# Performance work log

Measured on AMD Instinct MI355X. Metric: run time of the kernel, lower is better.

## Reference

```python
import jax, jax.numpy as jnp
import numpy as np

C = 0.1            # args.hyp_c
EPS_PROJ = 4e-3    # hyptorch project eps for float32
MIN_NORM = 1e-5
NUM_HEADS = 12


def _norm(x):
    return jnp.maximum(jnp.linalg.norm(x, axis=-1, keepdims=True), MIN_NORM)


def expmap0(u, c):
    sqrt_c = c ** 0.5
    u_norm = _norm(u)
    return jnp.tanh(sqrt_c * u_norm) * u / (sqrt_c * u_norm)


def project(x, c):
    sqrt_c = c ** 0.5
    norm = _norm(x)
    maxnorm = (1.0 - EPS_PROJ) / sqrt_c
    return jnp.where(norm > maxnorm, x / norm * maxnorm, x)


def logmap0(y, c):
    sqrt_c = c ** 0.5
    y_norm = _norm(y)
    arg = jnp.clip(sqrt_c * y_norm, -1 + 1e-5, 1 - 1e-5)
    artanh = 0.5 * jnp.log((1 + arg) / (1 - arg))
    return y / (y_norm * sqrt_c) * artanh


def qkv_attention(x, wq, bq, wk, bk, wv, bv, num_heads):
    # x: [B, N, D]; weights in torch Linear convention [out, in]
    B, N, D = x.shape
    dh = D // num_heads
    q = (x @ wq.T + bq).reshape(B, N, num_heads, dh)
    k = (x @ wk.T + bk).reshape(B, N, num_heads, dh)
    v = (x @ wv.T + bv).reshape(B, N, num_heads, dh)
    # NOTE: original has no 1/sqrt(dh) scaling — keep faithful
    att = jnp.einsum('bnhd,bmhd->bhnm', q, k)
    att = jax.nn.softmax(att, axis=-1)
    out = jnp.einsum('bhnm,bmhd->bnhd', att, v)
    return out.reshape(B, N, D)


def setup_inputs() -> dict:
    key = jax.random.key(0)
    ks = jax.random.split(key, 7)
    B, N, D = 8, 1024, 768
    s = 0.02
    return {
        'x':   jax.random.normal(ks[0], (B, N, D), jnp.float32),
        'w_q': jax.random.normal(ks[1], (3, D, D), jnp.float32) * s,
        'b_q': jax.random.normal(ks[2], (3, D), jnp.float32) * s,
        'w_k': jax.random.normal(ks[3], (3, D, D), jnp.float32) * s,
        'b_k': jax.random.normal(ks[4], (3, D), jnp.float32) * s,
        'w_v': jax.random.normal(ks[5], (3, D, D), jnp.float32) * s,
        'b_v': jax.random.normal(ks[6], (3, D), jnp.float32) * s,
    }


def reference(x, w_q, b_q, w_k, b_k, w_v, b_v):
    # branch 0: euclidean; branch 1: hyperbolic (ToPoincare); branch 2: spherical (FromPoincare)
    x_e = x
    x_h = project(expmap0(x, C), C)
    x_s = logmap0(x, C)
    out = 0.0
    for i, xb in enumerate((x_e, x_h, x_s)):
        out = out + qkv_attention(xb, w_q[i], b_q[i], w_k[i], b_k[i],
                                  w_v[i], b_v[i], NUM_HEADS)
    return out
```

## Files before the change

kernel.cpp:

```cpp
#include <hip/hip_runtime.h>
#include <hip/hip_bf16.h>
#include <cstdint>
#include <cstddef>

#define B_   8
#define N_   1024
#define D_   768
#define H_   12
#define DH_  64
#define M_   (B_ * N_)
#define WSZ_ (D_ * D_)

typedef __bf16 bf16;
typedef bf16  bf16x8  __attribute__((ext_vector_type(8)));
typedef bf16  bf16x4  __attribute__((ext_vector_type(4)));
typedef float floatx4 __attribute__((ext_vector_type(4)));

#define MFMA16 __builtin_amdgcn_mfma_f32_16x16x32_bf16

__device__ __forceinline__ float exp2_fast(float x) {
    float r;
    asm("v_exp_f32 %0, %1" : "=v"(r) : "v"(x));
    return r;
}

__device__ __forceinline__ void gload_lds16(const void* g, void* l) {
    __builtin_amdgcn_global_load_lds(
        (const __attribute__((address_space(1))) unsigned int*)g,
        (__attribute__((address_space(3))) unsigned int*)l, 16, 0, 0);
}

__global__ __launch_bounds__(256) void prep_x(const float* __restrict__ x,
                                              bf16* __restrict__ xbf,
                                              float* __restrict__ sc ) {
    int row = blockIdx.x;
    int tid = threadIdx.x;
    const float* xr = x + (size_t)row * D_;
    bf16* xo = xbf + (size_t)row * D_;
    float v0 = xr[tid], v1 = xr[tid + 256], v2 = xr[tid + 512];
    xo[tid]       = (bf16)v0;
    xo[tid + 256] = (bf16)v1;
    xo[tid + 512] = (bf16)v2;
    float ss = v0 * v0 + v1 * v1 + v2 * v2;
    for (int off = 32; off; off >>= 1) ss += __shfl_xor(ss, off, 64);
    __shared__ float red[4];
    if ((tid & 63) == 0) red[tid >> 6] = ss;
    __syncthreads();
    if (tid == 0) {
        float t2 = red[0] + red[1] + red[2] + red[3];
        float t  = sqrtf(t2);
        const float scst = 0.31622776601683794f;
        float un = fmaxf(t, 1e-5f);
        float s1 = tanhf(scst * un) / (scst * un);
        float nh = fmaxf(t * s1, 1e-5f);
        float maxnorm = (1.0f - 4e-3f) / scst;
        float sh = (nh > maxnorm) ? s1 * (maxnorm / nh) : s1;
        float arg = fminf(scst * un, 1.0f - 1e-5f);
        float artanh = 0.5f * logf((1.0f + arg) / (1.0f - arg));
        float ssc = artanh / (un * scst);
        sc[row]      = sh;
        sc[M_ + row] = ssc;
    }
}

__global__ __launch_bounds__(256) void prep_w(const float* __restrict__ wq,
                                              const float* __restrict__ wk,
                                              const float* __restrict__ wv,
                                              bf16* __restrict__ wbf) {
    size_t i = ((size_t)blockIdx.x * 256 + threadIdx.x) * 4;
    int z = (int)(i / WSZ_);
    int r = (int)(i % WSZ_);
    int branch = z / 3, t = z % 3;
    const float* src = (t == 0 ? wq : t == 1 ? wk : wv) + (size_t)branch * WSZ_ + r;
    float4 f = *(const float4*)src;
    bf16x4 o = { (bf16)f.x, (bf16)f.y, (bf16)f.z, (bf16)f.w };
    *(bf16x4*)(wbf + i) = o;
}

#define NT9 12

#define STG(buf, mat, half, t) do {                                          \
    const bf16* _src = (mat) ? wbf : xbf;                                    \
    int _rb = ((mat) ? bn0 : bm0) + (half) * 128 + w * 16 + (lane >> 2);     \
    const bf16* _g = _src + (size_t)_rb * D_ + (t) * 64 + (lane & 3) * 8;    \
    bf16* _l = &L[buf][mat][half][0][w * 16][0];                             \
    gload_lds16(_g, _l);                                                     \
    gload_lds16(_g + 32, _l + 4096);                                         \
} while (0)

#define LOADA(buf, mh) do {                                                  \
    _Pragma("unroll") for (int fi = 0; fi < 4; fi++)                         \
    _Pragma("unroll") for (int kk = 0; kk < 2; kk++)                         \
        afr[fi][kk] = *(const bf16x8*)(&L[buf][0][wm][kk][(mh)*64 + fi*16 + c15][quad*8]); \
} while (0)

#define LOADB(buf, nh) do {                                                  \
    _Pragma("unroll") for (int fj = 0; fj < 2; fj++)                         \
    _Pragma("unroll") for (int kk = 0; kk < 2; kk++)                         \
        bfr[nh][fj][kk] = *(const bf16x8*)(&L[buf][1][wn>>1][kk][(wn&1)*64 + (nh)*32 + fj*16 + c15][quad*8]); \
} while (0)

#define MFMACL(mh, nh) do {                                                  \
    __builtin_amdgcn_s_setprio(1);                                           \
    _Pragma("unroll") for (int fi = 0; fi < 4; fi++)                         \
    _Pragma("unroll") for (int fj = 0; fj < 2; fj++)                         \
    _Pragma("unroll") for (int kk = 0; kk < 2; kk++)                         \
        acc[(mh)*4 + fi][(nh)*2 + fj] =                                      \
            MFMA16(afr[fi][kk], bfr[nh][fj][kk], acc[(mh)*4 + fi][(nh)*2 + fj], 0, 0, 0); \
    __builtin_amdgcn_s_setprio(0);                                           \
} while (0)

#define BAR() __builtin_amdgcn_s_barrier()
#define VMW4() asm volatile("s_waitcnt vmcnt(4)" ::: "memory")

__global__ __launch_bounds__(512, 2) void gemm_qkv9(
        const bf16* __restrict__ xbf, const bf16* __restrict__ wbf,
        const float* __restrict__ bq, const float* __restrict__ bk,
        const float* __restrict__ bv, const float* __restrict__ sc,
        bf16* __restrict__ qkv) {
    int bid = blockIdx.x;
    int v = (bid & 7) * 108 + (bid >> 3);
    int bx = v >> 5;
    int by = v & 31;
    int bn0 = bx * 256;
    int bm0 = by * 256;

    __shared__ bf16 L[2][2][2][2][128][32];

    int tid = threadIdx.x;
    int w = tid >> 6, lane = tid & 63;
    int wm = w >> 2, wn = w & 3;
    int quad = lane >> 4, c15 = lane & 15;

    bf16x8 afr[4][2];
    bf16x8 bfr[2][2][2];
    floatx4 acc[8][4];
#pragma unroll
    for (int i = 0; i < 8; i++)
#pragma unroll
        for (int j = 0; j < 4; j++) acc[i][j] = (floatx4){0.f, 0.f, 0.f, 0.f};

    STG(0, 0, 0, 0); STG(0, 0, 1, 0); STG(0, 1, 0, 0); STG(0, 1, 1, 0);
    STG(1, 1, 0, 1); STG(1, 1, 1, 1);
    VMW4();
    BAR();

    for (int it = 0; it < 6; it++) {
        int t1 = 2 * it + 1;
        bool st2 = (it < 5);
        LOADA(0, 0); LOADB(0, 0);
        STG(1, 0, 0, t1);
        BAR(); MFMACL(0, 0); BAR();
        LOADB(0, 1);
        STG(1, 0, 1, t1);
        BAR(); MFMACL(0, 1); BAR();
        LOADA(0, 1);
        if (st2) STG(0, 1, 0, t1 + 1);
        BAR(); MFMACL(1, 1); BAR();
        if (st2) STG(0, 1, 1, t1 + 1);
        VMW4();
        BAR(); MFMACL(1, 0); BAR();
        LOADA(1, 0); LOADB(1, 0);
        if (st2) STG(0, 0, 0, t1 + 1);
        BAR(); MFMACL(0, 0); BAR();
        LOADB(1, 1);
        if (st2) STG(0, 0, 1, t1 + 1);
        BAR(); MFMACL(0, 1); BAR();
        LOADA(1, 1);
        if (st2) STG(1, 1, 0, t1 + 2);
        BAR(); MFMACL(1, 1); BAR();
        if (st2) STG(1, 1, 1, t1 + 2);
        VMW4();
        BAR(); MFMACL(1, 0); BAR();
    }

    int gz = bn0 / 768;
    int branch = gz / 3, t = gz % 3;
    int colz0 = (bn0 % 768) + wn * 64;
    const float* bias = (t == 0 ? bq : t == 1 ? bk : bv) + branch * D_;
    const float* scb = (branch == 0) ? nullptr : sc + (size_t)(branch - 1) * M_;
    float bj[4];
#pragma unroll
    for (int fj = 0; fj < 4; fj++) bj[fj] = bias[colz0 + fj * 16 + c15];
    bf16* outz = qkv + (size_t)gz * M_ * D_;
#pragma unroll
    for (int fi = 0; fi < 8; fi++) {
        int rowbase = bm0 + wm * 128 + fi * 16 + quad * 4;
        float4 sv = scb ? *(const float4*)(scb + rowbase)
                        : (float4){1.f, 1.f, 1.f, 1.f};
        float svr[4] = { sv.x, sv.y, sv.z, sv.w };
        if (t == 2) {
            int b = rowbase >> 10, nn = rowbase & 1023;
#pragma unroll
            for (int fj = 0; fj < 4; fj++) {
                int col = colz0 + fj * 16 + c15;
                int h = col >> 6, dd = col & 63;
                bf16x4 pkv;
#pragma unroll
                for (int r = 0; r < 4; r++)
                    pkv[r] = (bf16)(svr[r] * acc[fi][fj][r] + bj[fj]);
                *(bf16x4*)(outz + (((size_t)(b * H_ + h) * 64 + dd) << 10) + nn) = pkv;
            }
        } else {
#pragma unroll
            for (int r = 0; r < 4; r++) {
                bf16* orow = outz + (size_t)(rowbase + r) * D_;
#pragma unroll
                for (int fj = 0; fj < 4; fj++)
                    orow[colz0 + fj * 16 + c15] = (bf16)(svr[r] * acc[fi][fj][r] + bj[fj]);
            }
        }
    }
}

#define BM 128
#define BN 128
#define BK 32
__global__ __launch_bounds__(256) void gemm_qkv(
        const bf16* __restrict__ xbf, const bf16* __restrict__ wbf_all,
        const float* __restrict__ bq, const float* __restrict__ bk,
        const float* __restrict__ bv, const float* __restrict__ sc,
        int zoff, bf16* __restrict__ qkv) {
    int gz = zoff + blockIdx.z;
    int branch = gz / 3, t = gz % 3;
    const bf16*  wsrc = wbf_all + (size_t)gz * WSZ_;
    const float* bias = (t == 0 ? bq : t == 1 ? bk : bv) + branch * D_;
    bf16* out = qkv + (size_t)blockIdx.z * M_ * D_;
    int bm0 = blockIdx.y * BM;
    int bn0 = blockIdx.x * BN;

    __shared__ bf16 lA[BM * BK];
    __shared__ bf16 lB[BN * BK];

    int tid = threadIdx.x;
    int w = tid >> 6, lane = tid & 63;
    int wr = w >> 1, wc = w & 1;
    int quad = lane >> 4, c15 = lane & 15;
    int lrow = lane >> 2;
    int lcol = (lane & 3) * 8;

    floatx4 acc[4][4];
    for (int i = 0; i < 4; i++)
        for (int j = 0; j < 4; j++)
            acc[i][j] = (floatx4){0.f, 0.f, 0.f, 0.f};

    for (int k0 = 0; k0 < D_; k0 += BK) {
        const bf16* ga = xbf  + ((size_t)(bm0 + w * 32 + lrow) * D_ + k0 + lcol);
        const bf16* gb = wsrc + ((size_t)(bn0 + w * 32 + lrow) * D_ + k0 + lcol);
        gload_lds16(ga,           (char*)lA + w * 2048);
        gload_lds16(ga + 16 * D_, (char*)lA + w * 2048 + 1024);
        gload_lds16(gb,           (char*)lB + w * 2048);
        gload_lds16(gb + 16 * D_, (char*)lB + w * 2048 + 1024);
        __syncthreads();

        int arow = wr * 64 + c15;
        int brow = wc * 64 + c15;
        int kq = quad * 8;
        bf16x8 af[4], bfm[4];
        for (int i = 0; i < 4; i++) af[i]  = *(const bf16x8*)(lA + (arow + i * 16) * BK + kq);
        for (int j = 0; j < 4; j++) bfm[j] = *(const bf16x8*)(lB + (brow + j * 16) * BK + kq);
        for (int i = 0; i < 4; i++)
            for (int j = 0; j < 4; j++)
                acc[i][j] = MFMA16(af[i], bfm[j], acc[i][j], 0, 0, 0);
        __syncthreads();
    }

    const float* scb = (branch == 0) ? nullptr : sc + (size_t)(branch - 1) * M_;
    float bj[4];
    for (int j = 0; j < 4; j++) bj[j] = bias[bn0 + wc * 64 + j * 16 + c15];
    for (int i = 0; i < 4; i++) {
        int gRow0 = bm0 + wr * 64 + i * 16 + quad * 4;
        float s[4];
        for (int r = 0; r < 4; r++) s[r] = scb ? scb[gRow0 + r] : 1.0f;
        if (t == 2) {
            int b = gRow0 >> 10, nn = gRow0 & 1023;
            for (int j = 0; j < 4; j++) {
                int col = bn0 + wc * 64 + j * 16 + c15;
                int h = col >> 6, dd = col & 63;
                bf16x4 pkv;
                for (int r = 0; r < 4; r++)
                    pkv[r] = (bf16)(s[r] * acc[i][j][r] + bj[j]);
                *(bf16x4*)(out + (((size_t)(b * H_ + h) * 64 + dd) << 10) + nn) = pkv;
            }
        } else {
            for (int r = 0; r < 4; r++) {
                bf16* orow = out + (size_t)(gRow0 + r) * D_;
                for (int j = 0; j < 4; j++) {
                    int gCol = bn0 + wc * 64 + j * 16 + c15;
                    orow[gCol] = (bf16)(s[r] * acc[i][j][r] + bj[j]);
                }
            }
        }
    }
}

#define LDKP 72
__global__ __launch_bounds__(256) void attn(const bf16* __restrict__ qkv,
                                            float* __restrict__ out) {
    int qt = blockIdx.x;
    int bh = blockIdx.y;
    int br = blockIdx.z;
    int batch = bh / H_, head = bh % H_;
    int n0 = qt * 128;
    int tid = threadIdx.x, w = tid >> 6, lane = tid & 63;
    int quad = lane >> 4, c15 = lane & 15;

    const bf16* base = qkv + (size_t)br * 3 * M_ * D_;
    size_t baseRow = (size_t)batch * N_;
    int colOff = head * DH_;
    const bf16* qb  = base;
    const bf16* kb  = base + (size_t)M_ * D_;
    const bf16* vtb = base + (size_t)2 * M_ * D_
                    + ((size_t)(batch * H_ + head) * 64) * 1024;

    __shared__ bf16 sK[2][64][64];
    __shared__ bf16 sV[2][64][64];
    __shared__ bf16 sP[4][32 * LDKP];
    bf16* sPw = sP[w];

    int lr  = lane >> 3;
    int swz = ((lane & 7) ^ lr) * 8;
    const bf16* kgl = kb  + (baseRow + w * 8 + lr) * D_ + colOff + swz;
    const bf16* vgl = vtb + ((size_t)(w * 8 + lr)) * 1024 + swz;

    int s0 = (quad ^ (c15 & 7)) * 8;
    int s1 = s0 ^ 32;

    bf16x8 aq[2][2];
#pragma unroll
    for (int h = 0; h < 2; h++) {
        const bf16* qp = qb + ((baseRow + n0 + w * 32 + h * 16 + c15) * D_ + colOff + quad * 8);
        aq[h][0] = *(const bf16x8*)qp;
        aq[h][1] = *(const bf16x8*)(qp + 32);
#pragma unroll
        for (int f = 0; f < 2; f++)
#pragma unroll
            for (int i = 0; i < 8; i++)
                aq[h][f][i] = (bf16)((float)aq[h][f][i] * 1.4426950408889634f);
    }

    float m_sw[2] = { 0.f, 0.f };
    float l_sw[2] = { 0.f, 0.f };
    floatx4 o_acc[2][4];
#pragma unroll
    for (int h = 0; h < 2; h++)
#pragma unroll
        for (int j = 0; j < 4; j++) o_acc[h][j] = (floatx4){0.f, 0.f, 0.f, 0.f};

    gload_lds16(kgl,                      &sK[0][w * 8][0]);
    gload_lds16(kgl + (size_t)32 * D_,    &sK[0][32 + w * 8][0]);
    gload_lds16(vgl,                      &sV[0][w * 8][0]);
    gload_lds16(vgl + 32 * 1024,          &sV[0][32 + w * 8][0]);
    asm volatile("s_waitcnt vmcnt(0)" ::: "memory");
    __builtin_amdgcn_s_barrier();

    int buf = 0;
    for (int kt = 0; kt < 16; kt++) {
        if (kt < 15) {
            int m1 = (kt + 1) * 64;
            gload_lds16(kgl + (size_t)m1 * D_,        &sK[buf ^ 1][w * 8][0]);
            gload_lds16(kgl + (size_t)(m1 + 32) * D_, &sK[buf ^ 1][32 + w * 8][0]);
            gload_lds16(vgl + m1,                     &sV[buf ^ 1][w * 8][0]);
            gload_lds16(vgl + 32 * 1024 + m1,         &sV[buf ^ 1][32 + w * 8][0]);
        }

        floatx4 sfr[2][4];
        __builtin_amdgcn_s_setprio(1);
#pragma unroll
        for (int j = 0; j < 4; j++) {
            const bf16* kp = &sK[buf][j * 16 + c15][0];
            bf16x8 k0 = *(const bf16x8*)(kp + s0);
            bf16x8 k1 = *(const bf16x8*)(kp + s1);
#pragma unroll
            for (int h = 0; h < 2; h++) {
                floatx4 z = (floatx4){0.f, 0.f, 0.f, 0.f};
                z = MFMA16(k0, aq[h][0], z, 0, 0, 0);
                z = MFMA16(k1, aq[h][1], z, 0, 0, 0);
                sfr[h][j] = z;
            }
        }
        __builtin_amdgcn_s_setprio(0);

#pragma unroll
        for (int h = 0; h < 2; h++) {
            float q0 = fmaxf(fmaxf(sfr[h][0][0], sfr[h][0][1]), fmaxf(sfr[h][0][2], sfr[h][0][3]));
            float q1 = fmaxf(fmaxf(sfr[h][1][0], sfr[h][1][1]), fmaxf(sfr[h][1][2], sfr[h][1][3]));
            float q2 = fmaxf(fmaxf(sfr[h][2][0], sfr[h][2][1]), fmaxf(sfr[h][2][2], sfr[h][2][3]));
            float q3 = fmaxf(fmaxf(sfr[h][3][0], sfr[h][3][1]), fmaxf(sfr[h][3][2], sfr[h][3][3]));
            float mx = fmaxf(fmaxf(q0, q1), fmaxf(q2, q3));
            if (__any(mx > m_sw[h] + 11.0f)) {
                float mr = fmaxf(mx, __shfl_xor(mx, 16, 64));
                mr = fmaxf(mr, __shfl_xor(mr, 32, 64));
                float mnew = fmaxf(m_sw[h], mr);
                float alpha = exp2_fast(m_sw[h] - mnew);
                l_sw[h] *= alpha;
                m_sw[h] = mnew;
#pragma unroll
                for (int r = 0; r < 4; r++) {
                    float a = __shfl(alpha, quad * 4 + r, 64);
#pragma unroll
                    for (int j = 0; j < 4; j++) o_acc[h][j][r] *= a;
                }
            }
            float m = m_sw[h];
            float pe[4][4];
            bf16x4 pk[4];
#pragma unroll
            for (int j = 0; j < 4; j++)
#pragma unroll
                for (int r = 0; r < 4; r++) {
                    float p = exp2_fast(sfr[h][j][r] - m);
                    pe[j][r] = p;
                    pk[j][r] = (bf16)p;
                }
            float f0 = (pe[0][0] + pe[0][1]) + (pe[0][2] + pe[0][3]);
            float f1 = (pe[1][0] + pe[1][1]) + (pe[1][2] + pe[1][3]);
            float f2 = (pe[2][0] + pe[2][1]) + (pe[2][2] + pe[2][3]);
            float f3 = (pe[3][0] + pe[3][1]) + (pe[3][2] + pe[3][3]);
            float sum = (f0 + f1) + (f2 + f3);
            sum += __shfl_xor(sum, 16, 64);
            sum += __shfl_xor(sum, 32, 64);
            l_sw[h] += sum;
            bf16* pw = sPw + (h * 16 + c15) * LDKP;
#pragma unroll
            for (int j = 0; j < 4; j++)
                *(bf16x4*)(pw + j * 16 + quad * 4) = pk[j];
        }

        asm volatile("s_waitcnt lgkmcnt(0)" ::: "memory");
        __builtin_amdgcn_sched_barrier(0);

        bf16x8 ap[2][2];
#pragma unroll
        for (int h = 0; h < 2; h++) {
            const bf16* pp = sPw + (h * 16 + c15) * LDKP + quad * 8;
            ap[h][0] = *(const bf16x8*)pp;
            ap[h][1] = *(const bf16x8*)(pp + 32);
        }
        __builtin_amdgcn_s_setprio(1);
#pragma unroll
        for (int j = 0; j < 4; j++) {
            const bf16* vp = &sV[buf][j * 16 + c15][0];
            bf16x8 v0 = *(const bf16x8*)(vp + s0);
            bf16x8 v1 = *(const bf16x8*)(vp + s1);
#pragma unroll
            for (int h = 0; h < 2; h++) {
                o_acc[h][j] = MFMA16(ap[h][0], v0, o_acc[h][j], 0, 0, 0);
                o_acc[h][j] = MFMA16(ap[h][1], v1, o_acc[h][j], 0, 0, 0);
            }
        }
        __builtin_amdgcn_s_setprio(0);

        if (kt < 15) {
            asm volatile("s_waitcnt vmcnt(0)" ::: "memory");
            __builtin_amdgcn_s_barrier();
            buf ^= 1;
        }
    }

#pragma unroll
    for (int h = 0; h < 2; h++) {
        float inv = 1.0f / l_sw[h];
#pragma unroll
        for (int r = 0; r < 4; r++) {
            float iv = __shfl(inv, quad * 4 + r, 64);
            int row = n0 + w * 32 + h * 16 + quad * 4 + r;
            float* op = out + ((size_t)batch * N_ + row) * D_ + colOff;
#pragma unroll
            for (int j = 0; j < 4; j++) {
                float v = o_acc[h][j][r] * iv;
                int col = j * 16 + c15;
                unsafeAtomicAdd(op + col, v);
            }
        }
    }
}

extern "C" void kernel_launch(void* const* d_in, const int* in_sizes, int n_in,
                              void* d_out, int out_size, void* d_ws, size_t ws_size,
                              hipStream_t stream) {
    const float* x  = (const float*)d_in[0];
    const float* wq = (const float*)d_in[1];
    const float* bq = (const float*)d_in[2];
    const float* wk = (const float*)d_in[3];
    const float* bk = (const float*)d_in[4];
    const float* wv = (const float*)d_in[5];
    const float* bv = (const float*)d_in[6];
    float* out = (float*)d_out;

    char* ws = (char*)d_ws;
    bf16*  xbf = (bf16*)ws;
    bf16*  wbf = (bf16*)(ws + 12582912);
    float* sc  = (float*)(ws + 12582912 + 10616832);
    bf16*  qkv = (bf16*)(ws + 12582912 + 10616832 + 65536);

    const size_t matB = (size_t)M_ * D_ * 2;
    const size_t need_all = 12582912 + 10616832 + 65536 + 9 * matB;

    hipMemsetAsync(d_out, 0, out_size, stream);
    hipLaunchKernelGGL(prep_x, dim3(M_), dim3(256), 0, stream, x, xbf, sc);
    hipLaunchKernelGGL(prep_w, dim3((9 * WSZ_ / 4) / 256), dim3(256), 0, stream, wq, wk, wv, wbf);

    if (ws_size >= need_all) {
        hipLaunchKernelGGL(gemm_qkv9, dim3(864), dim3(512), 0, stream,
                           xbf, wbf, bq, bk, bv, sc, qkv);
        hipLaunchKernelGGL(attn, dim3(N_ / 128, B_ * H_, 3), dim3(256), 0, stream,
                           qkv, out);
    } else {
        for (int br = 0; br < 3; br++) {
            hipLaunchKernelGGL(gemm_qkv, dim3(D_ / BN, M_ / BM, 3), dim3(256), 0, stream,
                               xbf, wbf, bq, bk, bv, sc, br * 3, qkv);
            hipLaunchKernelGGL(attn, dim3(N_ / 128, B_ * H_, 1), dim3(256), 0, stream,
                               qkv, out);
        }
    }
}
```

Measured before the change: 362.8 us.

## Fuse three attention branches per block, drop memset and atomics

The attention kernel now loops over all three branches inside one block, using a continuous double-buffered K/V pipeline across branch boundaries. It sums the normalized outputs in registers and writes them with plain stores, which removes the output memset and the atomic adds in the main path. Blocks are remapped with an XCD-aware swizzle and launch bounds now request 4 waves per SIMD. prep_x also switches to float4 loads with 192 threads. In exchange, each block runs three times longer with a third as many blocks, and it holds more registers for the extra accumulator.

Result: slower. 385.2 us (+6.2%).

```diff
diff --git a/kernel.cpp b/kernel.cpp
--- a/kernel.cpp
+++ b/kernel.cpp
@@ -30,24 +30,22 @@
         (__attribute__((address_space(3))) unsigned int*)l, 16, 0, 0);
 }
 
-__global__ __launch_bounds__(256) void prep_x(const float* __restrict__ x,
+__global__ __launch_bounds__(192) void prep_x(const float* __restrict__ x,
                                               bf16* __restrict__ xbf,
                                               float* __restrict__ sc ) {
     int row = blockIdx.x;
     int tid = threadIdx.x;
     const float* xr = x + (size_t)row * D_;
-    bf16* xo = xbf + (size_t)row * D_;
-    float v0 = xr[tid], v1 = xr[tid + 256], v2 = xr[tid + 512];
-    xo[tid]       = (bf16)v0;
-    xo[tid + 256] = (bf16)v1;
-    xo[tid + 512] = (bf16)v2;
-    float ss = v0 * v0 + v1 * v1 + v2 * v2;
+    float4 v = *(const float4*)(xr + tid * 4);
+    bf16x4 o = { (bf16)v.x, (bf16)v.y, (bf16)v.z, (bf16)v.w };
+    *(bf16x4*)(xbf + (size_t)row * D_ + tid * 4) = o;
+    float ss = v.x * v.x + v.y * v.y + v.z * v.z + v.w * v.w;
     for (int off = 32; off; off >>= 1) ss += __shfl_xor(ss, off, 64);
-    __shared__ float red[4];
+    __shared__ float red[3];
     if ((tid & 63) == 0) red[tid >> 6] = ss;
     __syncthreads();
     if (tid == 0) {
-        float t2 = red[0] + red[1] + red[2] + red[3];
+        float t2 = red[0] + red[1] + red[2];
         float t  = sqrtf(t2);
         const float scst = 0.31622776601683794f;
         float un = fmaxf(t, 1e-5f);
@@ -295,23 +293,20 @@
 }
 
 #define LDKP 72
-__global__ __launch_bounds__(256) void attn(const bf16* __restrict__ qkv,
-                                            float* __restrict__ out) {
-    int qt = blockIdx.x;
-    int bh = blockIdx.y;
-    int br = blockIdx.z;
+__global__ __launch_bounds__(256, 4) void attn(const bf16* __restrict__ qkv,
+                                               float* __restrict__ out,
+                                               int nbr, int accumulate) {
+    int hwid = blockIdx.x;
+    int lg = (hwid & 7) * 96 + (hwid >> 3);
+    int qt = lg & 7;
+    int bh = lg >> 3;
     int batch = bh / H_, head = bh % H_;
     int n0 = qt * 128;
     int tid = threadIdx.x, w = tid >> 6, lane = tid & 63;
     int quad = lane >> 4, c15 = lane & 15;
 
-    const bf16* base = qkv + (size_t)br * 3 * M_ * D_;
     size_t baseRow = (size_t)batch * N_;
     int colOff = head * DH_;
-    const bf16* qb  = base;
-    const bf16* kb  = base + (size_t)M_ * D_;
-    const bf16* vtb = base + (size_t)2 * M_ * D_
-                    + ((size_t)(batch * H_ + head) * 64) * 1024;
 
     __shared__ bf16 sK[2][64][64];
     __shared__ bf16 sV[2][64][64];
@@ -320,48 +315,67 @@
 
     int lr  = lane >> 3;
     int swz = ((lane & 7) ^ lr) * 8;
-    const bf16* kgl = kb  + (baseRow + w * 8 + lr) * D_ + colOff + swz;
-    const bf16* vgl = vtb + ((size_t)(w * 8 + lr)) * 1024 + swz;
-
+    int stgRow = w * 8 + lr;
     int s0 = (quad ^ (c15 & 7)) * 8;
     int s1 = s0 ^ 32;
 
     bf16x8 aq[2][2];
-#pragma unroll
-    for (int h = 0; h < 2; h++) {
-        const bf16* qp = qb + ((baseRow + n0 + w * 32 + h * 16 + c15) * D_ + colOff + quad * 8);
-        aq[h][0] = *(const bf16x8*)qp;
-        aq[h][1] = *(const bf16x8*)(qp + 32);
-#pragma unroll
-        for (int f = 0; f < 2; f++)
-#pragma unroll
-            for (int i = 0; i < 8; i++)
-                aq[h][f][i] = (bf16)((float)aq[h][f][i] * 1.4426950408889634f);
-    }
-
-    float m_sw[2] = { 0.f, 0.f };
-    float l_sw[2] = { 0.f, 0.f };
+    float m_sw[2], l_sw[2];
     floatx4 o_acc[2][4];
+    floatx4 o_tot[2][4];
 #pragma unroll
     for (int h = 0; h < 2; h++)
 #pragma unroll
-        for (int j = 0; j < 4; j++) o_acc[h][j] = (floatx4){0.f, 0.f, 0.f, 0.f};
-
-    gload_lds16(kgl,                      &sK[0][w * 8][0]);
-    gload_lds16(kgl + (size_t)32 * D_,    &sK[0][32 + w * 8][0]);
-    gload_lds16(vgl,                      &sV[0][w * 8][0]);
-    gload_lds16(vgl + 32 * 1024,          &sV[0][32 + w * 8][0]);
-    asm volatile("s_waitcnt vmcnt(0)" ::: "memory");
-    __builtin_amdgcn_s_barrier();
+        for (int j = 0; j < 4; j++) o_tot[h][j] = (floatx4){0.f, 0.f, 0.f, 0.f};
+
+    {
+        const bf16* kg0 = qkv + (size_t)M_ * D_ + (baseRow + stgRow) * D_ + colOff + swz;
+        const bf16* vg0 = qkv + (size_t)2 * M_ * D_
+                        + ((size_t)(batch * H_ + head) * 64 + stgRow) * 1024 + swz;
+        gload_lds16(kg0,                   &sK[0][stgRow][0]);
+        gload_lds16(kg0 + (size_t)32 * D_, &sK[0][32 + stgRow][0]);
+        gload_lds16(vg0,                   &sV[0][stgRow][0]);
+        gload_lds16(vg0 + 32 * 1024,       &sV[0][32 + stgRow][0]);
+        asm volatile("s_waitcnt vmcnt(0)" ::: "memory");
+        __builtin_amdgcn_s_barrier();
+    }
 
     int buf = 0;
-    for (int kt = 0; kt < 16; kt++) {
-        if (kt < 15) {
-            int m1 = (kt + 1) * 64;
-            gload_lds16(kgl + (size_t)m1 * D_,        &sK[buf ^ 1][w * 8][0]);
-            gload_lds16(kgl + (size_t)(m1 + 32) * D_, &sK[buf ^ 1][32 + w * 8][0]);
-            gload_lds16(vgl + m1,                     &sV[buf ^ 1][w * 8][0]);
-            gload_lds16(vgl + 32 * 1024 + m1,         &sV[buf ^ 1][32 + w * 8][0]);
+    int tmax = 16 * nbr;
+    for (int t = 0; t < tmax; t++) {
+        int kt = t & 15;
+        if (kt == 0) {
+            int br = t >> 4;
+            const bf16* qp = qkv + (size_t)(br * 3) * M_ * D_
+                           + (baseRow + n0 + w * 32 + c15) * D_ + colOff + quad * 8;
+#pragma unroll
+            for (int h = 0; h < 2; h++) {
+                aq[h][0] = *(const bf16x8*)(qp + h * 16 * D_);
+                aq[h][1] = *(const bf16x8*)(qp + h * 16 * D_ + 32);
+#pragma unroll
+                for (int f = 0; f < 2; f++)
+#pragma unroll
+                    for (int i = 0; i < 8; i++)
+                        aq[h][f][i] = (bf16)((float)aq[h][f][i] * 1.4426950408889634f);
+            }
+            m_sw[0] = m_sw[1] = 0.f;
+            l_sw[0] = l_sw[1] = 0.f;
+#pragma unroll
+            for (int h = 0; h < 2; h++)
+#pragma unroll
+                for (int j = 0; j < 4; j++) o_acc[h][j] = (floatx4){0.f, 0.f, 0.f, 0.f};
+        }
+
+        if (t + 1 < tmax) {
+            int tn = t + 1, brn = tn >> 4, m1 = (tn & 15) * 64;
+            const bf16* kgn = qkv + (size_t)(brn * 3 + 1) * M_ * D_
+                            + (baseRow + m1 + stgRow) * D_ + colOff + swz;
+            const bf16* vgn = qkv + (size_t)(brn * 3 + 2) * M_ * D_
+                            + ((size_t)(batch * H_ + head) * 64 + stgRow) * 1024 + m1 + swz;
+            gload_lds16(kgn,                   &sK[buf ^ 1][stgRow][0]);
+            gload_lds16(kgn + (size_t)32 * D_, &sK[buf ^ 1][32 + stgRow][0]);
+            gload_lds16(vgn,                   &sV[buf ^ 1][stgRow][0]);
+            gload_lds16(vgn + 32 * 1024,       &sV[buf ^ 1][32 + stgRow][0]);
         }
 
         floatx4 sfr[2][4];
@@ -403,20 +417,19 @@
                 }
             }
             float m = m_sw[h];
-            float pe[4][4];
             bf16x4 pk[4];
 #pragma unroll
             for (int j = 0; j < 4; j++)
 #pragma unroll
                 for (int r = 0; r < 4; r++) {
                     float p = exp2_fast(sfr[h][j][r] - m);
-                    pe[j][r] = p;
+                    sfr[h][j][r] = p;
                     pk[j][r] = (bf16)p;
                 }
-            float f0 = (pe[0][0] + pe[0][1]) + (pe[0][2] + pe[0][3]);
-            float f1 = (pe[1][0] + pe[1][1]) + (pe[1][2] + pe[1][3]);
-            float f2 = (pe[2][0] + pe[2][1]) + (pe[2][2] + pe[2][3]);
-            float f3 = (pe[3][0] + pe[3][1]) + (pe[3][2] + pe[3][3]);
+            float f0 = (sfr[h][0][0] + sfr[h][0][1]) + (sfr[h][0][2] + sfr[h][0][3]);
+            float f1 = (sfr[h][1][0] + sfr[h][1][1]) + (sfr[h][1][2] + sfr[h][1][3]);
+            float f2 = (sfr[h][2][0] + sfr[h][2][1]) + (sfr[h][2][2] + sfr[h][2][3]);
+            float f3 = (sfr[h][3][0] + sfr[h][3][1]) + (sfr[h][3][2] + sfr[h][3][3]);
             float sum = (f0 + f1) + (f2 + f3);
             sum += __shfl_xor(sum, 16, 64);
             sum += __shfl_xor(sum, 32, 64);
@@ -451,7 +464,21 @@
         }
         __builtin_amdgcn_s_setprio(0);
 
-        if (kt < 15) {
+        if (kt == 15) {
+#pragma unroll
+            for (int h = 0; h < 2; h++) {
+                float inv = 1.0f / l_sw[h];
+#pragma unroll
+                for (int r = 0; r < 4; r++) {
+                    float iv = __shfl(inv, quad * 4 + r, 64);
+#pragma unroll
+                    for (int j = 0; j < 4; j++)
+                        o_tot[h][j][r] += o_acc[h][j][r] * iv;
+                }
+            }
+        }
+
+        if (t + 1 < tmax) {
             asm volatile("s_waitcnt vmcnt(0)" ::: "memory");
             __builtin_amdgcn_s_barrier();
             buf ^= 1;
@@ -460,17 +487,16 @@
 
 #pragma unroll
     for (int h = 0; h < 2; h++) {
-        float inv = 1.0f / l_sw[h];
 #pragma unroll
         for (int r = 0; r < 4; r++) {
-            float iv = __shfl(inv, quad * 4 + r, 64);
             int row = n0 + w * 32 + h * 16 + quad * 4 + r;
             float* op = out + ((size_t)batch * N_ + row) * D_ + colOff;
 #pragma unroll
             for (int j = 0; j < 4; j++) {
-                float v = o_acc[h][j][r] * iv;
+                float v = o_tot[h][j][r];
                 int col = j * 16 + c15;
-                unsafeAtomicAdd(op + col, v);
+                if (accumulate) unsafeAtomicAdd(op + col, v);
+                else            op[col] = v;
             }
         }
     }
@@ -497,21 +523,21 @@
     const size_t matB = (size_t)M_ * D_ * 2;
     const size_t need_all = 12582912 + 10616832 + 65536 + 9 * matB;
 
-    hipMemsetAsync(d_out, 0, out_size, stream);
-    hipLaunchKernelGGL(prep_x, dim3(M_), dim3(256), 0, stream, x, xbf, sc);
+    hipLaunchKernelGGL(prep_x, dim3(M_), dim3(192), 0, stream, x, xbf, sc);
     hipLaunchKernelGGL(prep_w, dim3((9 * WSZ_ / 4) / 256), dim3(256), 0, stream, wq, wk, wv, wbf);
 
     if (ws_size >= need_all) {
         hipLaunchKernelGGL(gemm_qkv9, dim3(864), dim3(512), 0, stream,
                            xbf, wbf, bq, bk, bv, sc, qkv);
-        hipLaunchKernelGGL(attn, dim3(N_ / 128, B_ * H_, 3), dim3(256), 0, stream,
-                           qkv, out);
+        hipLaunchKernelGGL(attn, dim3(768), dim3(256), 0, stream,
+                           qkv, out, 3, 0);
     } else {
+        hipMemsetAsync(d_out, 0, out_size, stream);
         for (int br = 0; br < 3; br++) {
             hipLaunchKernelGGL(gemm_qkv, dim3(D_ / BN, M_ / BM, 3), dim3(256), 0, stream,
                                xbf, wbf, bq, bk, bv, sc, br * 3, qkv);
-            hipLaunchKernelGGL(attn, dim3(N_ / 128, B_ * H_, 1), dim3(256), 0, stream,
-                               qkv, out);
-        }
-    }
-}
+            hipLaunchKernelGGL(attn, dim3(768), dim3(256), 0, stream,
+                               qkv, out, 1, 1);
+        }
+    }
+}
```

## Replace 256x256 QKV GEMM with 128x128 swizzled-LDS double-buffered kernel; vectorize prep_x

Applied to the files above, without the earlier changes.

Replaces the hand-scheduled 256x256-tile, 512-thread fused QKV GEMM with a simpler 128x128-tile, 256-thread kernel. The new kernel uses a BK=64 double buffer, XOR-swizzled LDS layout and one barrier per k-step, and launches four times as many blocks. The aim is to cut barrier overhead and LDS bank conflicts and to improve occupancy and load balance, at the cost of less data reuse per block. prep_x is also changed to use float4 loads with 192 threads per row.

New measurement: 385.9 us. +6.4%, slower.

```diff
diff --git a/kernel.cpp b/kernel.cpp
--- a/kernel.cpp
+++ b/kernel.cpp
@@ -30,24 +30,22 @@
         (__attribute__((address_space(3))) unsigned int*)l, 16, 0, 0);
 }
 
-__global__ __launch_bounds__(256) void prep_x(const float* __restrict__ x,
+__global__ __launch_bounds__(192) void prep_x(const float* __restrict__ x,
                                               bf16* __restrict__ xbf,
                                               float* __restrict__ sc ) {
     int row = blockIdx.x;
     int tid = threadIdx.x;
     const float* xr = x + (size_t)row * D_;
-    bf16* xo = xbf + (size_t)row * D_;
-    float v0 = xr[tid], v1 = xr[tid + 256], v2 = xr[tid + 512];
-    xo[tid]       = (bf16)v0;
-    xo[tid + 256] = (bf16)v1;
-    xo[tid + 512] = (bf16)v2;
-    float ss = v0 * v0 + v1 * v1 + v2 * v2;
+    float4 v = *(const float4*)(xr + tid * 4);
+    bf16x4 o = { (bf16)v.x, (bf16)v.y, (bf16)v.z, (bf16)v.w };
+    *(bf16x4*)(xbf + (size_t)row * D_ + tid * 4) = o;
+    float ss = v.x * v.x + v.y * v.y + v.z * v.z + v.w * v.w;
     for (int off = 32; off; off >>= 1) ss += __shfl_xor(ss, off, 64);
-    __shared__ float red[4];
+    __shared__ float red[3];
     if ((tid & 63) == 0) red[tid >> 6] = ss;
     __syncthreads();
     if (tid == 0) {
-        float t2 = red[0] + red[1] + red[2] + red[3];
+        float t2 = red[0] + red[1] + red[2];
         float t  = sqrtf(t2);
         const float scst = 0.31622776601683794f;
         float un = fmaxf(t, 1e-5f);
@@ -77,137 +75,114 @@
     *(bf16x4*)(wbf + i) = o;
 }
 
-#define NT9 12
-
-#define STG(buf, mat, half, t) do {                                          \
-    const bf16* _src = (mat) ? wbf : xbf;                                    \
-    int _rb = ((mat) ? bn0 : bm0) + (half) * 128 + w * 16 + (lane >> 2);     \
-    const bf16* _g = _src + (size_t)_rb * D_ + (t) * 64 + (lane & 3) * 8;    \
-    bf16* _l = &L[buf][mat][half][0][w * 16][0];                             \
-    gload_lds16(_g, _l);                                                     \
-    gload_lds16(_g + 32, _l + 4096);                                         \
-} while (0)
-
-#define LOADA(buf, mh) do {                                                  \
-    _Pragma("unroll") for (int fi = 0; fi < 4; fi++)                         \
-    _Pragma("unroll") for (int kk = 0; kk < 2; kk++)                         \
-        afr[fi][kk] = *(const bf16x8*)(&L[buf][0][wm][kk][(mh)*64 + fi*16 + c15][quad*8]); \
-} while (0)
-
-#define LOADB(buf, nh) do {                                                  \
-    _Pragma("unroll") for (int fj = 0; fj < 2; fj++)                         \
-    _Pragma("unroll") for (int kk = 0; kk < 2; kk++)                         \
-        bfr[nh][fj][kk] = *(const bf16x8*)(&L[buf][1][wn>>1][kk][(wn&1)*64 + (nh)*32 + fj*16 + c15][quad*8]); \
-} while (0)
-
-#define MFMACL(mh, nh) do {                                                  \
-    __builtin_amdgcn_s_setprio(1);                                           \
-    _Pragma("unroll") for (int fi = 0; fi < 4; fi++)                         \
-    _Pragma("unroll") for (int fj = 0; fj < 2; fj++)                         \
-    _Pragma("unroll") for (int kk = 0; kk < 2; kk++)                         \
-        acc[(mh)*4 + fi][(nh)*2 + fj] =                                      \
-            MFMA16(afr[fi][kk], bfr[nh][fj][kk], acc[(mh)*4 + fi][(nh)*2 + fj], 0, 0, 0); \
-    __builtin_amdgcn_s_setprio(0);                                           \
-} while (0)
-
-#define BAR() __builtin_amdgcn_s_barrier()
-#define VMW4() asm volatile("s_waitcnt vmcnt(4)" ::: "memory")
-
-__global__ __launch_bounds__(512, 2) void gemm_qkv9(
+__global__ __launch_bounds__(256, 2) void gemm128(
         const bf16* __restrict__ xbf, const bf16* __restrict__ wbf,
         const float* __restrict__ bq, const float* __restrict__ bk,
         const float* __restrict__ bv, const float* __restrict__ sc,
         bf16* __restrict__ qkv) {
     int bid = blockIdx.x;
-    int v = (bid & 7) * 108 + (bid >> 3);
-    int bx = v >> 5;
-    int by = v & 31;
-    int bn0 = bx * 256;
-    int bm0 = by * 256;
-
-    __shared__ bf16 L[2][2][2][2][128][32];
+    int v = (bid & 7) * 432 + (bid >> 3);
+    int bx = v >> 6;
+    int by = v & 63;
+    int bn0g = bx * 128;
+    int bm0  = by * 128;
+
+    __shared__ bf16 LA[2][128][64];
+    __shared__ bf16 LB[2][128][64];
 
     int tid = threadIdx.x;
     int w = tid >> 6, lane = tid & 63;
-    int wm = w >> 2, wn = w & 3;
+    int wr = w >> 1, wc = w & 1;
     int quad = lane >> 4, c15 = lane & 15;
-
-    bf16x8 afr[4][2];
-    bf16x8 bfr[2][2][2];
-    floatx4 acc[8][4];
-#pragma unroll
-    for (int i = 0; i < 8; i++)
+    int lr = lane >> 3;
+    int gsw = ((lane & 7) ^ lr) * 8;
+
+    const bf16* asrc = xbf + (size_t)bm0 * D_;
+    const bf16* wsrc = wbf + (size_t)bn0g * D_;
+
+    floatx4 acc[4][4];
+#pragma unroll
+    for (int i = 0; i < 4; i++)
 #pragma unroll
         for (int j = 0; j < 4; j++) acc[i][j] = (floatx4){0.f, 0.f, 0.f, 0.f};
 
-    STG(0, 0, 0, 0); STG(0, 0, 1, 0); STG(0, 1, 0, 0); STG(0, 1, 1, 0);
-    STG(1, 1, 0, 1); STG(1, 1, 1, 1);
-    VMW4();
-    BAR();
-
-    for (int it = 0; it < 6; it++) {
-        int t1 = 2 * it + 1;
-        bool st2 = (it < 5);
-        LOADA(0, 0); LOADB(0, 0);
-        STG(1, 0, 0, t1);
-        BAR(); MFMACL(0, 0); BAR();
-        LOADB(0, 1);
-        STG(1, 0, 1, t1);
-        BAR(); MFMACL(0, 1); BAR();
-        LOADA(0, 1);
-        if (st2) STG(0, 1, 0, t1 + 1);
-        BAR(); MFMACL(1, 1); BAR();
-        if (st2) STG(0, 1, 1, t1 + 1);
-        VMW4();
-        BAR(); MFMACL(1, 0); BAR();
-        LOADA(1, 0); LOADB(1, 0);
-        if (st2) STG(0, 0, 0, t1 + 1);
-        BAR(); MFMACL(0, 0); BAR();
-        LOADB(1, 1);
-        if (st2) STG(0, 0, 1, t1 + 1);
-        BAR(); MFMACL(0, 1); BAR();
-        LOADA(1, 1);
-        if (st2) STG(1, 1, 0, t1 + 2);
-        BAR(); MFMACL(1, 1); BAR();
-        if (st2) STG(1, 1, 1, t1 + 2);
-        VMW4();
-        BAR(); MFMACL(1, 0); BAR();
-    }
-
-    int gz = bn0 / 768;
-    int branch = gz / 3, t = gz % 3;
-    int colz0 = (bn0 % 768) + wn * 64;
-    const float* bias = (t == 0 ? bq : t == 1 ? bk : bv) + branch * D_;
+#define G128(buf, t) do {                                                     \
+    _Pragma("unroll") for (int c = 0; c < 4; c++) {                           \
+        int rr = c * 32 + w * 8;                                              \
+        gload_lds16(asrc + (size_t)(rr + lr) * D_ + (t) * 64 + gsw,           \
+                    &LA[buf][rr][0]);                                         \
+        gload_lds16(wsrc + (size_t)(rr + lr) * D_ + (t) * 64 + gsw,           \
+                    &LB[buf][rr][0]);                                         \
+    }                                                                         \
+} while (0)
+
+    G128(0, 0);
+    asm volatile("s_waitcnt vmcnt(0)" ::: "memory");
+    __builtin_amdgcn_s_barrier();
+
+    int buf = 0;
+    for (int t = 0; t < 12; t++) {
+        if (t < 11) G128(buf ^ 1, t + 1);
+#pragma unroll
+        for (int kk = 0; kk < 2; kk++) {
+            int sA = ((kk * 4 + quad) ^ (c15 & 7)) * 8;
+            bf16x8 af[4], bfm[4];
+#pragma unroll
+            for (int i = 0; i < 4; i++)
+                af[i] = *(const bf16x8*)(&LA[buf][wr * 64 + i * 16 + c15][sA]);
+#pragma unroll
+            for (int j = 0; j < 4; j++)
+                bfm[j] = *(const bf16x8*)(&LB[buf][wc * 64 + j * 16 + c15][sA]);
+            __builtin_amdgcn_s_setprio(1);
+#pragma unroll
+            for (int i = 0; i < 4; i++)
+#pragma unroll
+                for (int j = 0; j < 4; j++)
+                    acc[i][j] = MFMA16(af[i], bfm[j], acc[i][j], 0, 0, 0);
+            __builtin_amdgcn_s_setprio(0);
+        }
+        if (t < 11) {
+            asm volatile("s_waitcnt vmcnt(0)" ::: "memory");
+            __builtin_amdgcn_s_barrier();
+            buf ^= 1;
+        }
+    }
+#undef G128
+
+    int gz = bn0g / 768;
+    int branch = gz / 3, tmat = gz % 3;
+    int coll0 = (bn0g % 768) + wc * 64;
+    const float* bias = (tmat == 0 ? bq : tmat == 1 ? bk : bv) + branch * D_;
     const float* scb = (branch == 0) ? nullptr : sc + (size_t)(branch - 1) * M_;
     float bj[4];
 #pragma unroll
-    for (int fj = 0; fj < 4; fj++) bj[fj] = bias[colz0 + fj * 16 + c15];
+    for (int j = 0; j < 4; j++) bj[j] = bias[coll0 + j * 16 + c15];
     bf16* outz = qkv + (size_t)gz * M_ * D_;
 #pragma unroll
-    for (int fi = 0; fi < 8; fi++) {
-        int rowbase = bm0 + wm * 128 + fi * 16 + quad * 4;
-        float4 sv = scb ? *(const float4*)(scb + rowbase)
-                        : (float4){1.f, 1.f, 1.f, 1.f};
-        float svr[4] = { sv.x, sv.y, sv.z, sv.w };
-        if (t == 2) {
-            int b = rowbase >> 10, nn = rowbase & 1023;
-#pragma unroll
-            for (int fj = 0; fj < 4; fj++) {
-                int col = colz0 + fj * 16 + c15;
+    for (int i = 0; i < 4; i++) {
+        int gRow0 = bm0 + wr * 64 + i * 16 + quad * 4;
+        float s[4];
+#pragma unroll
+        for (int r = 0; r < 4; r++) s[r] = scb ? scb[gRow0 + r] : 1.0f;
+        if (tmat == 2) {
+            int b = gRow0 >> 10, nn = gRow0 & 1023;
+#pragma unroll
+            for (int j = 0; j < 4; j++) {
+                int col = coll0 + j * 16 + c15;
                 int h = col >> 6, dd = col & 63;
                 bf16x4 pkv;
 #pragma unroll
                 for (int r = 0; r < 4; r++)
-                    pkv[r] = (bf16)(svr[r] * acc[fi][fj][r] + bj[fj]);
+                    pkv[r] = (bf16)(s[r] * acc[i][j][r] + bj[j]);
                 *(bf16x4*)(outz + (((size_t)(b * H_ + h) * 64 + dd) << 10) + nn) = pkv;
             }
         } else {
 #pragma unroll
             for (int r = 0; r < 4; r++) {
-                bf16* orow = outz + (size_t)(rowbase + r) * D_;
-#pragma unroll
-                for (int fj = 0; fj < 4; fj++)
-                    orow[colz0 + fj * 16 + c15] = (bf16)(svr[r] * acc[fi][fj][r] + bj[fj]);
+                bf16* orow = outz + (size_t)(gRow0 + r) * D_;
+#pragma unroll
+                for (int j = 0; j < 4; j++)
+                    orow[coll0 + j * 16 + c15] = (bf16)(s[r] * acc[i][j][r] + bj[j]);
             }
         }
     }
@@ -498,11 +473,11 @@
     const size_t need_all = 12582912 + 10616832 + 65536 + 9 * matB;
 
     hipMemsetAsync(d_out, 0, out_size, stream);
-    hipLaunchKernelGGL(prep_x, dim3(M_), dim3(256), 0, stream, x, xbf, sc);
+    hipLaunchKernelGGL(prep_x, dim3(M_), dim3(192), 0, stream, x, xbf, sc);
     hipLaunchKernelGGL(prep_w, dim3((9 * WSZ_ / 4) / 256), dim3(256), 0, stream, wq, wk, wv, wbf);
 
     if (ws_size >= need_all) {
-        hipLaunchKernelGGL(gemm_qkv9, dim3(864), dim3(512), 0, stream,
+        hipLaunchKernelGGL(gemm128, dim3(3456), dim3(256), 0, stream,
                            xbf, wbf, bq, bk, bv, sc, qkv);
         hipLaunchKernelGGL(attn, dim3(N_ / 128, B_ * H_, 3), dim3(256), 0, stream,
                            qkv, out);
```

## Shrink attention P staging to one 16-row XOR-swizzled tile, vectorize prep_x

Applied to the files above, without the earlier changes.

The attention kernel now stages P for one 16-row half at a time in a smaller XOR-swizzled shared buffer instead of a padded 32-row buffer. It hoists the V fragment loads ahead of softmax and interleaves each half's PV MFMAs with the other half's softmax work. It also sets launch bounds requesting 4 blocks per CU, which cuts LDS and may raise occupancy but adds register pressure from the hoisted V fragments. prep_x switches to 192 threads with float4 loads and bf16x4 stores.

After: 422.7 us. 16.5% more time.

```diff
diff --git a/kernel.cpp b/kernel.cpp
--- a/kernel.cpp
+++ b/kernel.cpp
@@ -30,24 +30,22 @@
         (__attribute__((address_space(3))) unsigned int*)l, 16, 0, 0);
 }
 
-__global__ __launch_bounds__(256) void prep_x(const float* __restrict__ x,
+__global__ __launch_bounds__(192) void prep_x(const float* __restrict__ x,
                                               bf16* __restrict__ xbf,
                                               float* __restrict__ sc ) {
     int row = blockIdx.x;
     int tid = threadIdx.x;
     const float* xr = x + (size_t)row * D_;
-    bf16* xo = xbf + (size_t)row * D_;
-    float v0 = xr[tid], v1 = xr[tid + 256], v2 = xr[tid + 512];
-    xo[tid]       = (bf16)v0;
-    xo[tid + 256] = (bf16)v1;
-    xo[tid + 512] = (bf16)v2;
-    float ss = v0 * v0 + v1 * v1 + v2 * v2;
+    float4 v = *(const float4*)(xr + tid * 4);
+    bf16x4 o = { (bf16)v.x, (bf16)v.y, (bf16)v.z, (bf16)v.w };
+    *(bf16x4*)(xbf + (size_t)row * D_ + tid * 4) = o;
+    float ss = v.x * v.x + v.y * v.y + v.z * v.z + v.w * v.w;
     for (int off = 32; off; off >>= 1) ss += __shfl_xor(ss, off, 64);
-    __shared__ float red[4];
+    __shared__ float red[3];
     if ((tid & 63) == 0) red[tid >> 6] = ss;
     __syncthreads();
     if (tid == 0) {
-        float t2 = red[0] + red[1] + red[2] + red[3];
+        float t2 = red[0] + red[1] + red[2];
         float t  = sqrtf(t2);
         const float scst = 0.31622776601683794f;
         float un = fmaxf(t, 1e-5f);
@@ -294,9 +292,8 @@
     }
 }
 
-#define LDKP 72
-__global__ __launch_bounds__(256) void attn(const bf16* __restrict__ qkv,
-                                            float* __restrict__ out) {
+__global__ __launch_bounds__(256, 4) void attn(const bf16* __restrict__ qkv,
+                                               float* __restrict__ out) {
     int qt = blockIdx.x;
     int bh = blockIdx.y;
     int br = blockIdx.z;
@@ -315,8 +312,7 @@
 
     __shared__ bf16 sK[2][64][64];
     __shared__ bf16 sV[2][64][64];
-    __shared__ bf16 sP[4][32 * LDKP];
-    bf16* sPw = sP[w];
+    __shared__ bf16 sP[4][16][64];
 
     int lr  = lane >> 3;
     int swz = ((lane & 7) ^ lr) * 8;
@@ -325,6 +321,7 @@
 
     int s0 = (quad ^ (c15 & 7)) * 8;
     int s1 = s0 ^ 32;
+    int spx = (c15 & 7) * 8;
 
     bf16x8 aq[2][2];
 #pragma unroll
@@ -380,6 +377,14 @@
             }
         }
         __builtin_amdgcn_s_setprio(0);
+
+        bf16x8 vf0[4], vf1[4];
+#pragma unroll
+        for (int j = 0; j < 4; j++) {
+            const bf16* vp = &sV[buf][j * 16 + c15][0];
+            vf0[j] = *(const bf16x8*)(vp + s0);
+            vf1[j] = *(const bf16x8*)(vp + s1);
+        }
 
 #pragma unroll
         for (int h = 0; h < 2; h++) {
@@ -421,35 +426,25 @@
             sum += __shfl_xor(sum, 16, 64);
             sum += __shfl_xor(sum, 32, 64);
             l_sw[h] += sum;
-            bf16* pw = sPw + (h * 16 + c15) * LDKP;
+
+            bf16* pw = &sP[w][c15][0];
 #pragma unroll
             for (int j = 0; j < 4; j++)
-                *(bf16x4*)(pw + j * 16 + quad * 4) = pk[j];
-        }
-
-        asm volatile("s_waitcnt lgkmcnt(0)" ::: "memory");
-        __builtin_amdgcn_sched_barrier(0);
-
-        bf16x8 ap[2][2];
-#pragma unroll
-        for (int h = 0; h < 2; h++) {
-            const bf16* pp = sPw + (h * 16 + c15) * LDKP + quad * 8;
-            ap[h][0] = *(const bf16x8*)pp;
-            ap[h][1] = *(const bf16x8*)(pp + 32);
-        }
-        __builtin_amdgcn_s_setprio(1);
-#pragma unroll
-        for (int j = 0; j < 4; j++) {
-            const bf16* vp = &sV[buf][j * 16 + c15][0];
-            bf16x8 v0 = *(const bf16x8*)(vp + s0);
-            bf16x8 v1 = *(const bf16x8*)(vp + s1);
-#pragma unroll
-            for (int h = 0; h < 2; h++) {
-                o_acc[h][j] = MFMA16(ap[h][0], v0, o_acc[h][j], 0, 0, 0);
-                o_acc[h][j] = MFMA16(ap[h][1], v1, o_acc[h][j], 0, 0, 0);
-            }
-        }
-        __builtin_amdgcn_s_setprio(0);
+                *(bf16x4*)(pw + (((j * 16 + quad * 4)) ^ spx)) = pk[j];
+
+            asm volatile("s_waitcnt lgkmcnt(0)" ::: "memory");
+            __builtin_amdgcn_sched_barrier(0);
+
+            bf16x8 ap0 = *(const bf16x8*)(pw + ((quad * 8) ^ spx));
+            bf16x8 ap1 = *(const bf16x8*)(pw + ((32 + quad * 8) ^ spx));
+            __builtin_amdgcn_s_setprio(1);
+#pragma unroll
+            for (int j = 0; j < 4; j++) {
+                o_acc[h][j] = MFMA16(ap0, vf0[j], o_acc[h][j], 0, 0, 0);
+                o_acc[h][j] = MFMA16(ap1, vf1[j], o_acc[h][j], 0, 0, 0);
+            }
+            __builtin_amdgcn_s_setprio(0);
+        }
 
         if (kt < 15) {
             asm volatile("s_waitcnt vmcnt(0)" ::: "memory");
@@ -498,7 +493,7 @@
     const size_t need_all = 12582912 + 10616832 + 65536 + 9 * matB;
 
     hipMemsetAsync(d_out, 0, out_size, stream);
-    hipLaunchKernelGGL(prep_x, dim3(M_), dim3(256), 0, stream, x, xbf, sc);
+    hipLaunchKernelGGL(prep_x, dim3(M_), dim3(192), 0, stream, x, xbf, sc);
     hipLaunchKernelGGL(prep_w, dim3((9 * WSZ_ / 4) / 256), dim3(256), 0, stream, wq, wk, wv, wbf);
 
     if (ws_size >= need_all) {
```
